# Performance work log

Hardware: AMD Instinct MI355X
Metric: run time of the kernel (lower is better)

## Reference

```python
import jax, jax.numpy as jnp
import numpy as np

B, D, LC, LQ = 16, 128, 2048, 256
NEG = jnp.float32(-1e30)


def setup_inputs() -> dict:
    key = jax.random.key(0)
    k1, k2, k3, k4, k5, k6, k7 = jax.random.split(key, 7)
    C = jax.random.normal(k1, (B, D, LC), dtype=jnp.float32)
    Q = jax.random.normal(k2, (B, D, LQ), dtype=jnp.float32)
    cmask = jax.random.randint(k3, (B, LC), 0, 2, dtype=jnp.int32)
    qmask = jax.random.randint(k4, (B, LQ), 0, 2, dtype=jnp.int32)
    # learned params: trilinear projection vector and resizer linear
    w = jax.random.normal(k5, (3 * D,), dtype=jnp.float32) * (1.0 / np.sqrt(3 * D))
    W_res = jax.random.normal(k6, (D, 4 * D), dtype=jnp.float32) * np.sqrt(2.0 / (4 * D))
    b_res = jnp.zeros((D,), dtype=jnp.float32)
    return {"C": C, "Q": Q, "cmask": cmask, "qmask": qmask,
            "w": w, "W_res": W_res, "b_res": b_res}


def reference(C, Q, cmask, qmask, w, W_res, b_res):
    # C: [B,D,Lc], Q: [B,D,Lq] -> work in [B,L,D] layout
    Ct = jnp.swapaxes(C, 1, 2)  # [B,Lc,D]
    Qt = jnp.swapaxes(Q, 1, 2)  # [B,Lq,D]
    d = Ct.shape[-1]
    w1, w2, w3 = w[:d], w[d:2 * d], w[2 * d:]
    # trilinear similarity S[b,i,j] = Ct_i.w1 + Qt_j.w2 + (Ct_i*Qt_j).w3
    # equivalent to matmul(cat(Ct,Qt,Ct*Qt), w) without materializing [B,Lc,Lq,3D]
    S = (jnp.einsum('bid,d->bi', Ct, w1)[:, :, None]
         + jnp.einsum('bjd,d->bj', Qt, w2)[:, None, :]
         + jnp.einsum('bid,bjd->bij', Ct * w3, Qt))  # [B,Lc,Lq]
    qm = qmask.astype(jnp.float32)[:, None, :]  # [B,1,Lq]
    cm = cmask.astype(jnp.float32)[:, :, None]  # [B,Lc,1]
    S_row = jax.nn.softmax(S + NEG * (1.0 - qm), axis=2)   # softmax over Lq
    S_col = jax.nn.softmax(S + NEG * (1.0 - cm), axis=1)   # softmax over Lc
    A = jnp.einsum('bij,bjd->bid', S_row, Qt)               # [B,Lc,D]
    # (S_row @ S_col^T) @ C computed as S_row @ (S_col^T @ C)
    ScTC = jnp.einsum('bkj,bkd->bjd', S_col, Ct)            # [B,Lq,D]
    Bm = jnp.einsum('bij,bjd->bid', S_row, ScTC)            # [B,Lc,D]
    out = jnp.concatenate((Ct, A, Ct * A, Ct * Bm), axis=2)  # [B,Lc,4D]
    out = jax.nn.relu(jnp.einsum('bif,df->bid', out, W_res) + b_res)
    return jnp.swapaxes(out, 1, 2)  # [B,D,Lc]
```

## Files before the change

### kernel.cpp

```cpp
#include <hip/hip_runtime.h>


#define B_ 16
#define D_ 128
#define LC_ 2048
#define LQ_ 256
#define NEGV -1e30f

typedef float f4 __attribute__((ext_vector_type(4)));
typedef float f32x4 __attribute__((ext_vector_type(4)));
typedef short bfrag __attribute__((ext_vector_type(8)));
typedef unsigned short us4 __attribute__((ext_vector_type(4)));

__device__ __forceinline__ unsigned short f2b(float x) {
    unsigned u = __float_as_uint(x);
    u += 0x7fff + ((u >> 16) & 1);
    return (unsigned short)(u >> 16);
}

__device__ __forceinline__ float b2f(short s) {
    return __uint_as_float(((unsigned)(unsigned short)s) << 16);
}

__device__ __forceinline__ void gld16(const void* g, void* l) {
    __builtin_amdgcn_global_load_lds(
        (const __attribute__((address_space(1))) unsigned*)g,
        (__attribute__((address_space(3))) unsigned*)l, 16, 0, 0);
}

__global__ __launch_bounds__(256) void k_prep(const float* __restrict__ C,
        const float* __restrict__ Q, const float* __restrict__ w,
        const int* __restrict__ cmask, const int* __restrict__ qmask,
        const float* __restrict__ W_res,
        unsigned short* __restrict__ Cbf, unsigned short* __restrict__ Cwt,
        unsigned short* __restrict__ Qt, unsigned short* __restrict__ Mb,
        unsigned short* __restrict__ Wb, float* __restrict__ rC,
        float* __restrict__ rQ) {
    __shared__ float T[128][64];
    __shared__ float red[4][64];
    int tid = threadIdx.x;
    if (blockIdx.x < 512) {
        int b = blockIdx.x >> 5, i0 = (blockIdx.x & 31) * 64;
        int ii = tid & 63, db = tid >> 6;
        if (tid < 128) {
            int wo = blockIdx.x * 128 + tid;
            Wb[wo] = f2b(W_res[wo]);
        }
#pragma unroll
        for (int k = 0; k < 32; ++k) {
            int dd = db + 4 * k;
            float raw = C[((size_t)b * D_ + dd) * LC_ + i0 + ii];
            T[dd][ii] = raw;
            Cbf[((size_t)b * D_ + dd) * LC_ + i0 + ii] = f2b(raw);
        }
        __syncthreads();
        {
            float p = 0.f;
#pragma unroll
            for (int k = 0; k < 32; ++k) p += w[db * 32 + k] * T[db * 32 + k][ii];
            red[db][ii] = p;
        }
        int dq = db * 32;
#pragma unroll
        for (int m = 0; m < 8; ++m) {
            us4 v;
#pragma unroll
            for (int e = 0; e < 4; ++e) {
                int d = dq + m * 4 + e;
                v[e] = f2b(w[2 * D_ + d] * T[d][ii]);
            }
            *(us4*)&Cwt[((size_t)(b * LC_ + i0 + ii)) * D_ + dq + m * 4] = v;
        }
        __syncthreads();
        if (tid < 64) {
            int gi = b * LC_ + i0 + tid;
            rC[gi] = red[0][tid] + red[1][tid] + red[2][tid] + red[3][tid]
                   + (cmask[gi] ? 0.f : NEGV);
        }
    } else {
        int bq = blockIdx.x - 512;
        int b = bq >> 2, j0 = (bq & 3) * 64;
        int jj = tid & 63, db = tid >> 6;
#pragma unroll
        for (int k = 0; k < 32; ++k) {
            int dd = db + 4 * k;
            float raw = Q[((size_t)b * D_ + dd) * LQ_ + j0 + jj];
            T[dd][jj] = raw;
            Mb[((size_t)(b * 256 + dd)) * LQ_ + j0 + jj] = f2b(raw);
        }
        __syncthreads();
        {
            float p = 0.f;
#pragma unroll
            for (int k = 0; k < 32; ++k) p += w[D_ + db * 32 + k] * T[db * 32 + k][jj];
            red[db][jj] = p;
        }
        int dq = db * 32;
#pragma unroll
        for (int m = 0; m < 8; ++m) {
            us4 v;
#pragma unroll
            for (int e = 0; e < 4; ++e) v[e] = f2b(T[dq + m * 4 + e][jj]);
            *(us4*)&Qt[((size_t)(b * LQ_ + j0 + jj)) * D_ + dq + m * 4] = v;
        }
        __syncthreads();
        if (tid < 64) {
            int gj = b * LQ_ + j0 + tid;
            rQ[gj] = red[0][tid] + red[1][tid] + red[2][tid] + red[3][tid]
                   + (qmask[gj] ? 0.f : NEGV);
        }
    }
}

__global__ __launch_bounds__(256) void k_sctcmm(
        const unsigned short* __restrict__ Qt, const unsigned short* __restrict__ Cwt,
        const float* __restrict__ rcm, const unsigned short* __restrict__ Cbf,
        float* __restrict__ part, float* __restrict__ paz) {
    __shared__ __align__(16) unsigned short QJ[64 * 128];
    __shared__ __align__(16) unsigned short CW[64 * 128];
    __shared__ __align__(16) unsigned short Cs[128 * 64];
    int bid = blockIdx.x;
    int ks = bid & 3, jt = (bid >> 2) & 3, b = bid >> 4;
    int j0 = jt * 64;
    int tid = threadIdx.x, wv = tid >> 6, lane = tid & 63;
    int jw = wv & 1, dw = wv >> 1;
    int l15 = lane & 15, q = lane >> 4;

#pragma unroll
    for (int t = 0; t < 4; ++t) {
        int G = t * 256 + tid;
        int j = G >> 4, g = G & 15;
        gld16(Qt + ((size_t)(b * LQ_ + j0 + j)) * D_ + ((g ^ (j & 7)) << 3), &QJ[G * 8]);
    }

    f32x4 acc[2][4];
#pragma unroll
    for (int mm = 0; mm < 2; ++mm)
#pragma unroll
        for (int nn = 0; nn < 4; ++nn) acc[mm][nn] = (f32x4){0.f, 0.f, 0.f, 0.f};
    float zac[4] = {0.f, 0.f, 0.f, 0.f};

    for (int c = 0; c < 8; ++c) {
        int ic = ks * 512 + c * 64;
        __syncthreads();
#pragma unroll
        for (int t = 0; t < 4; ++t) {
            int G = t * 256 + tid;
            int i = G >> 4, g = G & 15;
            gld16(Cwt + ((size_t)(b * LC_ + ic + i)) * D_ + ((g ^ (i & 7)) << 3), &CW[G * 8]);
        }
#pragma unroll
        for (int t = 0; t < 4; ++t) {
            int G = t * 256 + tid;
            int d = G >> 3, g = G & 7;
            gld16(Cbf + ((size_t)(b * D_ + d)) * LC_ + ic + ((g ^ (d & 7)) << 3), &Cs[G * 8]);
        }
        __syncthreads();
        f32x4 sacc[4];
#pragma unroll
        for (int n = 0; n < 4; ++n) sacc[n] = (f32x4){0.f, 0.f, 0.f, 0.f};
#pragma unroll
        for (int ksd = 0; ksd < 4; ++ksd) {
            int jr = wv * 16 + l15;
            bfrag av = *(const bfrag*)&QJ[jr * 128 + (((ksd * 4 + q) ^ (jr & 7)) << 3)];
#pragma unroll
            for (int n = 0; n < 4; ++n) {
                int ir = n * 16 + l15;
                bfrag bv = *(const bfrag*)&CW[ir * 128 + (((ksd * 4 + q) ^ (ir & 7)) << 3)];
                sacc[n] = __builtin_amdgcn_mfma_f32_16x16x32_bf16(av, bv, sacc[n], 0, 0, 0);
            }
        }
        __syncthreads();
#pragma unroll
        for (int n = 0; n < 4; ++n) {
            int i = n * 16 + l15;
            float rc = rcm[b * LC_ + ic + i];
#pragma unroll
            for (int r = 0; r < 4; ++r) {
                int j = wv * 16 + q * 4 + r;
                float e = __expf(sacc[n][r] + rc);
                zac[r] += e;
                *(unsigned short*)((char*)CW + j * 128 +
                    (((i >> 3) ^ (j & 7)) << 4) + (i & 7) * 2) = f2b(e);
            }
        }
        __syncthreads();
#pragma unroll
        for (int kk = 0; kk < 2; ++kk) {
            bfrag afr[2];
#pragma unroll
            for (int mm = 0; mm < 2; ++mm) {
                int j = jw * 32 + mm * 16 + l15;
                afr[mm] = *(const bfrag*)((const char*)CW + j * 128 +
                    (((kk * 4 + q) ^ (j & 7)) << 4));
            }
#pragma unroll
            for (int nn = 0; nn < 4; ++nn) {
                int d = dw * 64 + nn * 16 + l15;
                int g = kk * 4 + q;
                bfrag bv = *(const bfrag*)&Cs[d * 64 + ((g ^ (d & 7)) << 3)];
#pragma unroll
                for (int mm = 0; mm < 2; ++mm)
                    acc[mm][nn] = __builtin_amdgcn_mfma_f32_16x16x32_bf16(afr[mm], bv, acc[mm][nn], 0, 0, 0);
            }
        }
    }
#pragma unroll
    for (int r = 0; r < 4; ++r) {
        zac[r] += __shfl_xor(zac[r], 1, 64);
        zac[r] += __shfl_xor(zac[r], 2, 64);
        zac[r] += __shfl_xor(zac[r], 4, 64);
        zac[r] += __shfl_xor(zac[r], 8, 64);
    }
    if (l15 == 0) {
#pragma unroll
        for (int r = 0; r < 4; ++r)
            paz[((size_t)(ks * B_ + b)) * LQ_ + j0 + wv * 16 + q * 4 + r] = zac[r];
    }
#pragma unroll
    for (int mm = 0; mm < 2; ++mm)
#pragma unroll
        for (int nn = 0; nn < 4; ++nn) {
            int d = dw * 64 + nn * 16 + l15;
#pragma unroll
            for (int r = 0; r < 4; ++r) {
                int j = j0 + jw * 32 + mm * 16 + q * 4 + r;
                part[((size_t)(ks * B_ + b) * LQ_ + j) * D_ + d] = acc[mm][nn][r];
            }
        }
}

__global__ __launch_bounds__(256) void k_red(const float* __restrict__ part,
        const float* __restrict__ paz, unsigned short* __restrict__ Mb) {
    __shared__ float Ts[64][68];
    int bid = blockIdx.x;
    int dt = bid & 1, jt = (bid >> 1) & 3, b = bid >> 3;
    int j0 = jt * 64, d0 = dt * 64;
    int tid = threadIdx.x;
    {
        int jj = tid >> 2, dq = (tid & 3) * 16;
        float zs = paz[((size_t)(0 * B_ + b)) * LQ_ + j0 + jj]
                 + paz[((size_t)(1 * B_ + b)) * LQ_ + j0 + jj]
                 + paz[((size_t)(2 * B_ + b)) * LQ_ + j0 + jj]
                 + paz[((size_t)(3 * B_ + b)) * LQ_ + j0 + jj];
        float rz = 1.0f / zs;
        f4 s[4];
#pragma unroll
        for (int q = 0; q < 4; ++q) s[q] = (f4){0.f, 0.f, 0.f, 0.f};
#pragma unroll
        for (int ks = 0; ks < 4; ++ks) {
            size_t base = ((size_t)(ks * B_ + b) * LQ_ + j0 + jj) * D_ + d0 + dq;
#pragma unroll
            for (int q = 0; q < 4; ++q) s[q] += *(const f4*)&part[base + q * 4];
        }
#pragma unroll
        for (int q = 0; q < 4; ++q) {
            f4 v = {s[q][0] * rz, s[q][1] * rz, s[q][2] * rz, s[q][3] * rz};
            *(f4*)&Ts[jj][dq + q * 4] = v;
        }
    }
    __syncthreads();
    {
        int dd = tid >> 2, jq = (tid & 3) * 16;
        us4 o0, o1, o2, o3;
#pragma unroll
        for (int q = 0; q < 4; ++q) o0[q] = f2b(Ts[jq + q][dd]);
#pragma unroll
        for (int q = 0; q < 4; ++q) o1[q] = f2b(Ts[jq + 4 + q][dd]);
#pragma unroll
        for (int q = 0; q < 4; ++q) o2[q] = f2b(Ts[jq + 8 + q][dd]);
#pragma unroll
        for (int q = 0; q < 4; ++q) o3[q] = f2b(Ts[jq + 12 + q][dd]);
        unsigned short* dst = Mb + ((size_t)(b * 256 + 128 + d0 + dd)) * LQ_ + j0 + jq;
        *(us4*)&dst[0] = o0; *(us4*)&dst[4] = o1; *(us4*)&dst[8] = o2; *(us4*)&dst[12] = o3;
    }
}

__global__ __launch_bounds__(256, 2) void k_rowproj(
        const unsigned short* __restrict__ Qt, const unsigned short* __restrict__ Cwt,
        const float* __restrict__ rQm, const unsigned short* __restrict__ Mb,
        const unsigned short* __restrict__ Cbf, const unsigned short* __restrict__ Wb,
        const float* __restrict__ bres, float* __restrict__ outp) {
    __shared__ __align__(16) unsigned short L[32768];
    unsigned short* QA   = L;
    unsigned short* Ps   = L;
    unsigned short* Ms   = L + 16384;
    float*          Zp   = (float*)(L + 16384);
    unsigned short* F    = L;
    unsigned short* WsL  = L + 16384;
    unsigned short* CbfL = L + 24576;

    int bid = blockIdx.x;
    int swz = (bid & 7) * 64 + (bid >> 3);
    int b = swz >> 5, i0 = (swz & 31) * 64;
    int tid = threadIdx.x, wv = tid >> 6, lane = tid & 63;
    int l15 = lane & 15, q = lane >> 4;

#pragma unroll
    for (int k = 0; k < 16; ++k) {
        int G = k * 256 + tid;
        int j = G >> 4, g = G & 15;
        gld16(Qt + ((size_t)(b * LQ_ + j)) * D_ + ((g ^ (j & 7)) << 3), &QA[G * 8]);
    }
    __syncthreads();
    f32x4 sacc[4][4];
#pragma unroll
    for (int m = 0; m < 4; ++m)
#pragma unroll
        for (int n = 0; n < 4; ++n) sacc[m][n] = (f32x4){0.f, 0.f, 0.f, 0.f};
#pragma unroll
    for (int ksd = 0; ksd < 4; ++ksd) {
        bfrag bv[4];
#pragma unroll
        for (int n = 0; n < 4; ++n)
            bv[n] = *(const bfrag*)&Cwt[
                ((size_t)(b * LC_ + i0 + n * 16 + l15)) * D_ + ksd * 32 + q * 8];
        bfrag av[4];
#pragma unroll
        for (int m = 0; m < 4; ++m) {
            int jr = wv * 64 + m * 16 + l15;
            av[m] = *(const bfrag*)&QA[jr * 128 + (((ksd * 4 + q) ^ (jr & 7)) << 3)];
        }
        __builtin_amdgcn_s_setprio(1);
#pragma unroll
        for (int m = 0; m < 4; ++m)
#pragma unroll
            for (int n = 0; n < 4; ++n)
                sacc[m][n] = __builtin_amdgcn_mfma_f32_16x16x32_bf16(av[m], bv[n], sacc[m][n], 0, 0, 0);
        __builtin_amdgcn_s_setprio(0);
    }
    __syncthreads();
    float zp[4] = {0.f, 0.f, 0.f, 0.f};
#pragma unroll
    for (int m = 0; m < 4; ++m) {
        f4 rq4 = *(const f4*)&rQm[b * LQ_ + wv * 64 + m * 16 + q * 4];
#pragma unroll
        for (int n = 0; n < 4; ++n) {
            int i = n * 16 + l15;
#pragma unroll
            for (int r = 0; r < 4; ++r) {
                int j = wv * 64 + m * 16 + q * 4 + r;
                float e = __expf(sacc[m][n][r] + rq4[r]);
                zp[n] += e;
                *(unsigned short*)((char*)Ps + i * 512 +
                    (((j >> 3) ^ (i & 7)) << 4) + (j & 7) * 2) = f2b(e);
            }
        }
    }
#pragma unroll
    for (int n = 0; n < 4; ++n) {
        zp[n] += __shfl_xor(zp[n], 16, 64);
        zp[n] += __shfl_xor(zp[n], 32, 64);
    }
    if (q == 0) {
#pragma unroll
        for (int n = 0; n < 4; ++n) Zp[wv * 64 + n * 16 + l15] = zp[n];
    }
    __syncthreads();
    float rzv[4][4];
#pragma unroll
    for (int m = 0; m < 4; ++m)
#pragma unroll
        for (int r = 0; r < 4; ++r) {
            int i = m * 16 + q * 4 + r;
            rzv[m][r] = 1.f / (Zp[i] + Zp[64 + i] + Zp[128 + i] + Zp[192 + i]);
        }

    f32x4 acc[4][4];
#pragma unroll
    for (int m = 0; m < 4; ++m)
#pragma unroll
        for (int n = 0; n < 4; ++n) acc[m][n] = (f32x4){0.f, 0.f, 0.f, 0.f};
    for (int jc = 0; jc < 4; ++jc) {
        __syncthreads();
#pragma unroll
        for (int t = 0; t < 8; ++t) {
            int G = t * 256 + tid;
            int c = G >> 3, g = G & 7;
            gld16(Mb + ((size_t)(b * 256 + c)) * LQ_ + jc * 64 + ((g ^ (c & 7)) << 3),
                  &Ms[G * 8]);
        }
        __syncthreads();
        __builtin_amdgcn_s_setprio(1);
#pragma unroll
        for (int kk = 0; kk < 2; ++kk) {
            bfrag av[4];
#pragma unroll
            for (int m = 0; m < 4; ++m) {
                int row = m * 16 + l15;
                int gp = (jc * 8 + kk * 4 + q) ^ (row & 7);
                av[m] = *(const bfrag*)((const char*)Ps + row * 512 + (gp << 4));
            }
#pragma unroll
            for (int n = 0; n < 4; ++n) {
                int c = wv * 64 + n * 16 + l15;
                int gb = (kk * 4 + q) ^ (c & 7);
                bfrag bv = *(const bfrag*)((const char*)Ms + c * 128 + (gb << 4));
#pragma unroll
                for (int m = 0; m < 4; ++m)
                    acc[m][n] = __builtin_amdgcn_mfma_f32_16x16x32_bf16(av[m], bv, acc[m][n], 0, 0, 0);
            }
        }
        __builtin_amdgcn_s_setprio(0);
    }

    __syncthreads();
#pragma unroll
    for (int t = 0; t < 4; ++t) {
        int G = t * 256 + tid;
        int d = G >> 3, g = G & 7;
        gld16(Cbf + ((size_t)(b * D_ + d)) * LC_ + i0 + ((g ^ (d & 7)) << 3), &CbfL[G * 8]);
    }
    __syncthreads();

    f32x4 pacc[4][2];
#pragma unroll
    for (int m = 0; m < 4; ++m)
#pragma unroll
        for (int n = 0; n < 2; ++n) pacc[m][n] = (f32x4){0.f, 0.f, 0.f, 0.f};
    int wr = wv >> 1, wc = wv & 1;

#pragma unroll
    for (int fh = 0; fh < 2; ++fh) {
        if (fh == 0) {
            if (wv < 2) {
#pragma unroll
                for (int m = 0; m < 4; ++m) {
                    int ibase = m * 16 + q * 4;
#pragma unroll
                    for (int n = 0; n < 4; ++n) {
                        int fc = 128 + wv * 64 + n * 16 + l15;
#pragma unroll
                        for (int r = 0; r < 4; ++r) {
                            int i = ibase + r;
                            *(unsigned short*)((char*)F + i * 512 +
                                (((fc >> 3) ^ (i & 7)) << 4) + (fc & 7) * 2)
                                = f2b(acc[m][n][r] * rzv[m][r]);
                        }
                    }
                }
            } else {
#pragma unroll
                for (int m = 0; m < 4; ++m) {
#pragma unroll
                    for (int n = 0; n < 4; ++n) {
                        int d = (wv - 2) * 64 + n * 16 + l15;
#pragma unroll
                        for (int r = 0; r < 4; ++r) {
                            int i = m * 16 + q * 4 + r;
                            unsigned short cv = *(const unsigned short*)((const char*)CbfL +
                                d * 128 + (((i >> 3) ^ (d & 7)) << 4) + (i & 7) * 2);
                            *(unsigned short*)((char*)F + i * 512 +
                                (((d >> 3) ^ (i & 7)) << 4) + (d & 7) * 2) = cv;
                        }
                    }
                }
            }
        } else {
#pragma unroll
            for (int m = 0; m < 4; ++m) {
                int ibase = m * 16 + q * 4;
#pragma unroll
                for (int n = 0; n < 4; ++n) {
                    int c = wv * 64 + n * 16 + l15;
                    int d = c & 127;
#pragma unroll
                    for (int r = 0; r < 4; ++r) {
                        int i = ibase + r;
                        float ct = b2f((short)*(const unsigned short*)((const char*)CbfL +
                            d * 128 + (((i >> 3) ^ (d & 7)) << 4) + (i & 7) * 2));
                        *(unsigned short*)((char*)F + i * 512 +
                            (((c >> 3) ^ (i & 7)) << 4) + (c & 7) * 2)
                            = f2b(ct * acc[m][n][r] * rzv[m][r]);
                    }
                }
            }
        }
        __syncthreads();
#pragma unroll
        for (int kc = 0; kc < 4; ++kc) {
#pragma unroll
            for (int t = 0; t < 4; ++t) {
                int G = t * 256 + tid;
                int d = G >> 3, g = G & 7;
                gld16(Wb + (size_t)d * 512 + fh * 256 + kc * 64 + ((g ^ (d & 7)) << 3),
                      &WsL[G * 8]);
            }
            __syncthreads();
            __builtin_amdgcn_s_setprio(1);
#pragma unroll
            for (int kk = 0; kk < 2; ++kk) {
                bfrag av[4];
#pragma unroll
                for (int m = 0; m < 4; ++m) {
                    int d = wr * 64 + m * 16 + l15;
                    av[m] = *(const bfrag*)((const char*)WsL + d * 128 +
                        (((kk * 4 + q) ^ (d & 7)) << 4));
                }
#pragma unroll
                for (int n = 0; n < 2; ++n) {
                    int i = wc * 32 + n * 16 + l15;
                    int gf = kc * 8 + kk * 4 + q;
                    bfrag bv = *(const bfrag*)((const char*)F + i * 512 +
                        ((gf ^ (i & 7)) << 4));
#pragma unroll
                    for (int m = 0; m < 4; ++m)
                        pacc[m][n] = __builtin_amdgcn_mfma_f32_16x16x32_bf16(av[m], bv, pacc[m][n], 0, 0, 0);
                }
            }
            __builtin_amdgcn_s_setprio(0);
            __syncthreads();
        }
    }
#pragma unroll
    for (int m = 0; m < 4; ++m) {
        int dbase = wr * 64 + m * 16 + q * 4;
        f4 bias = *(const f4*)&bres[dbase];
#pragma unroll
        for (int n = 0; n < 2; ++n) {
            int i = i0 + wc * 32 + n * 16 + l15;
#pragma unroll
            for (int r = 0; r < 4; ++r) {
                float v = pacc[m][n][r] + bias[r];
                outp[((size_t)(b * D_ + dbase + r)) * LC_ + i] = fmaxf(v, 0.f);
            }
        }
    }
}

extern "C" void kernel_launch(void* const* d_in, const int* in_sizes, int n_in,
                              void* d_out, int out_size, void* d_ws, size_t ws_size,
                              hipStream_t stream) {
    const float* C = (const float*)d_in[0];
    const float* Q = (const float*)d_in[1];
    const int* cmask = (const int*)d_in[2];
    const int* qmask = (const int*)d_in[3];
    const float* w = (const float*)d_in[4];
    const float* W_res = (const float*)d_in[5];
    const float* b_res = (const float*)d_in[6];
    float* out = (float*)d_out;
    float* ws = (float*)d_ws;

    float* rC    = ws;
    float* rQ    = rC + 32768;
    float* paz   = rQ + 4096;
    float* part  = paz + 16384;
    float* wbf_f = part + (size_t)2097152;
    float* mb_f  = wbf_f + 32768;
    float* cbf_f = mb_f + 524288;
    float* cwt_f = cbf_f + (size_t)2097152;
    float* qt_f  = cwt_f + (size_t)2097152;

    unsigned short* Wb  = (unsigned short*)wbf_f;
    unsigned short* Mb  = (unsigned short*)mb_f;
    unsigned short* Cbf = (unsigned short*)cbf_f;
    unsigned short* Cwt = (unsigned short*)cwt_f;
    unsigned short* Qt  = (unsigned short*)qt_f;

    k_prep<<<576, 256, 0, stream>>>(C, Q, w, cmask, qmask, W_res,
                                    Cbf, Cwt, Qt, Mb, Wb, rC, rQ);
    k_sctcmm<<<B_ * 16, 256, 0, stream>>>(Qt, Cwt, rC, Cbf, part, paz);
    k_red<<<B_ * 8, 256, 0, stream>>>(part, paz, Mb);
    k_rowproj<<<B_ * 32, 256, 0, stream>>>(Qt, Cwt, rQ, Mb, Cbf, Wb, b_res, out);
}
```

Before: 66.15 us.

## Double-buffer C chunk staging in k_sctcmm to overlap loads with MFMA

The CW and Cs shared-memory tiles in the S_col^T·C kernel become two buffers each. The next 64-column chunk is issued into the idle buffer while the current chunk is computed, and one barrier per iteration replaces the load, barrier, compute pattern. The goal is to hide global-to-LDS latency behind the MFMA work. In exchange, LDS use per block rises to roughly 80 KB, which can lower occupancy. The existing mid-loop barrier may also force the outstanding prefetch to complete early, which would limit the overlap.

After: 67.08 us. No clear change (+1.4%).

```diff
diff --git a/kernel.cpp b/kernel.cpp
--- a/kernel.cpp
+++ b/kernel.cpp
@@ -117,8 +117,8 @@
         const float* __restrict__ rcm, const unsigned short* __restrict__ Cbf,
         float* __restrict__ part, float* __restrict__ paz) {
     __shared__ __align__(16) unsigned short QJ[64 * 128];
-    __shared__ __align__(16) unsigned short CW[64 * 128];
-    __shared__ __align__(16) unsigned short Cs[128 * 64];
+    __shared__ __align__(16) unsigned short CWb[2][64 * 128];
+    __shared__ __align__(16) unsigned short Csb[2][128 * 64];
     int bid = blockIdx.x;
     int ks = bid & 3, jt = (bid >> 2) & 3, b = bid >> 4;
     int j0 = jt * 64;
@@ -126,12 +126,32 @@
     int jw = wv & 1, dw = wv >> 1;
     int l15 = lane & 15, q = lane >> 4;
 
+#define STAGE_CHUNK(cc, CWdst, Csdst)                                              \
+    do {                                                                            \
+        int ic_ = ks * 512 + (cc) * 64;                                             \
+        _Pragma("unroll")                                                           \
+        for (int t = 0; t < 4; ++t) {                                               \
+            int G = t * 256 + tid;                                                  \
+            int i_ = G >> 4, g_ = G & 15;                                           \
+            gld16(Cwt + ((size_t)(b * LC_ + ic_ + i_)) * D_ + ((g_ ^ (i_ & 7)) << 3), \
+                  &(CWdst)[G * 8]);                                                 \
+        }                                                                           \
+        _Pragma("unroll")                                                           \
+        for (int t = 0; t < 4; ++t) {                                               \
+            int G = t * 256 + tid;                                                  \
+            int d_ = G >> 3, g_ = G & 7;                                            \
+            gld16(Cbf + ((size_t)(b * D_ + d_)) * LC_ + ic_ + ((g_ ^ (d_ & 7)) << 3), \
+                  &(Csdst)[G * 8]);                                                 \
+        }                                                                           \
+    } while (0)
+
 #pragma unroll
     for (int t = 0; t < 4; ++t) {
         int G = t * 256 + tid;
         int j = G >> 4, g = G & 15;
         gld16(Qt + ((size_t)(b * LQ_ + j0 + j)) * D_ + ((g ^ (j & 7)) << 3), &QJ[G * 8]);
     }
+    STAGE_CHUNK(0, CWb[0], Csb[0]);
 
     f32x4 acc[2][4];
 #pragma unroll
@@ -140,22 +160,14 @@
         for (int nn = 0; nn < 4; ++nn) acc[mm][nn] = (f32x4){0.f, 0.f, 0.f, 0.f};
     float zac[4] = {0.f, 0.f, 0.f, 0.f};
 
+    __syncthreads();
+
     for (int c = 0; c < 8; ++c) {
+        int cur = c & 1;
+        unsigned short* CW = CWb[cur];
+        unsigned short* Cs = Csb[cur];
         int ic = ks * 512 + c * 64;
-        __syncthreads();
-#pragma unroll
-        for (int t = 0; t < 4; ++t) {
-            int G = t * 256 + tid;
-            int i = G >> 4, g = G & 15;
-            gld16(Cwt + ((size_t)(b * LC_ + ic + i)) * D_ + ((g ^ (i & 7)) << 3), &CW[G * 8]);
-        }
-#pragma unroll
-        for (int t = 0; t < 4; ++t) {
-            int G = t * 256 + tid;
-            int d = G >> 3, g = G & 7;
-            gld16(Cbf + ((size_t)(b * D_ + d)) * LC_ + ic + ((g ^ (d & 7)) << 3), &Cs[G * 8]);
-        }
-        __syncthreads();
+        if (c < 7) STAGE_CHUNK(c + 1, CWb[cur ^ 1], Csb[cur ^ 1]);
         f32x4 sacc[4];
 #pragma unroll
         for (int n = 0; n < 4; ++n) sacc[n] = (f32x4){0.f, 0.f, 0.f, 0.f};
@@ -204,7 +216,9 @@
                     acc[mm][nn] = __builtin_amdgcn_mfma_f32_16x16x32_bf16(afr[mm], bv, acc[mm][nn], 0, 0, 0);
             }
         }
-    }
+        __syncthreads();
+    }
+#undef STAGE_CHUNK
 #pragma unroll
     for (int r = 0; r < 4; ++r) {
         zac[r] += __shfl_xor(zac[r], 1, 64);
```
